# Kernel tuning notes

Hardware: AMD Instinct MI355X
Metric: run time of the kernel (lower is better)

The kernel has to match this reference:

```python
import jax, jax.numpy as jnp
import numpy as np
import math

H, W = 1024, 1280
NUM_CLASSES = 81  # 80 foreground + background
CENTER_VAR, SIZE_VAR = 0.1, 0.2
CONF_THR, NMS_THR = 0.01, 0.45
PRE_NMS_K, MAX_DET = 400, 100

def make_priors():
    strides_x = [32, 64, 128, 213, 320]
    strides_y = [32, 64, 128, 256, 512]
    fmx = [int(W / s) for s in strides_x]
    fmy = [int(H / s) for s in strides_y]
    expand = H / 256.0
    mins = [10 * expand, 62 * expand, 114 * expand, 166 * expand, 218 * expand]
    maxs = [62 * expand, 114 * expand, 166 * expand, 218 * expand, 270 * expand]
    ars = [[2, 3], [2, 3], [2, 3], [2], [2]]
    pri = []
    for k in range(5):
        for i in range(fmy[k]):
            for j in range(fmx[k]):
                cx = (j + 0.5) / fmx[k]
                cy = (i + 0.5) / fmy[k]
                pri.append([cx, cy, mins[k] / W, mins[k] / H])
                s = math.sqrt(mins[k] * maxs[k])
                pri.append([cx, cy, s / W, s / H])
                for r in ars[k]:
                    sr = math.sqrt(r)
                    pri.append([cx, cy, mins[k] * sr / W, mins[k] / sr / H])
                    pri.append([cx, cy, mins[k] / sr / W, mins[k] * sr / H])
    return np.clip(np.asarray(pri, np.float32), 0.0, 1.0)  # [P,4] center form

def setup_inputs():
    key = jax.random.key(0)
    k1, k2 = jax.random.split(key)
    pri = jnp.asarray(make_priors())  # [10208, 4]
    P = pri.shape[0]
    return {
        "cls_logits": jax.random.normal(k1, (32, P, NUM_CLASSES), jnp.float32),
        "bbox_pred": jax.random.normal(k2, (32, P, 4), jnp.float32) * 0.5,
        "priors": pri,
    }

def _decode(loc, priors):
    # convert_locations_to_boxes: center-form decode with variances
    c = loc[..., :2] * CENTER_VAR * priors[..., 2:] + priors[..., :2]
    s = jnp.exp(loc[..., 2:] * SIZE_VAR) * priors[..., 2:]
    # center_form_to_corner_form
    return jnp.concatenate([c - s * 0.5, c + s * 0.5], axis=-1)

def _iou(a, b):
    lt = jnp.maximum(a[:, None, :2], b[None, :, :2])
    rb = jnp.minimum(a[:, None, 2:], b[None, :, 2:])
    wh = jnp.clip(rb - lt, 0.0)
    inter = wh[..., 0] * wh[..., 1]
    ar = (a[:, 2] - a[:, 0]) * (a[:, 3] - a[:, 1])
    br = (b[:, 2] - b[:, 0]) * (b[:, 3] - b[:, 1])
    return inter / (ar[:, None] + br[None, :] - inter + 1e-9)

def _post_one(scores, boxes):
    # scores: [P, C] softmax probs, boxes: [P, 4] corner form in [0,1]
    C = scores.shape[1]
    fg = scores[:, 1:]  # drop background
    bx = boxes * jnp.asarray([W, H, W, H], boxes.dtype)  # scale to image coords
    topv, topi = jax.lax.top_k(fg.reshape(-1), PRE_NMS_K)  # pre-NMS candidates
    prior_idx = topi // (C - 1)
    cls = topi % (C - 1) + 1
    cb = bx[prior_idx]  # [K,4]
    # class-aware (batched) NMS: offset boxes by class so classes never overlap
    off = cls.astype(bx.dtype)[:, None] * float(max(H, W) + 1)
    ob = cb + off
    iou = _iou(ob, ob)  # [K,K]
    keep0 = topv > CONF_THR
    idx = jnp.arange(PRE_NMS_K)
    def body(keep, i):
        sup = (iou[i] > NMS_THR) & (idx > i) & keep[i]
        return keep & ~sup, None
    keep, _ = jax.lax.scan(body, keep0, jnp.arange(PRE_NMS_K))
    sc = jnp.where(keep, topv, 0.0)
    fv, fi = jax.lax.top_k(sc, MAX_DET)
    return cb[fi], cls[fi], fv  # boxes [100,4], labels [100], scores [100]

def reference(cls_logits, bbox_pred, priors):
    scores = jax.nn.softmax(cls_logits, axis=2)  # [B,P,C]
    boxes = _decode(bbox_pred, priors)           # [B,P,4]
    return jax.vmap(_post_one)(scores, boxes)
```

## Files before the change

kernel.cpp:

```cpp
#include <hip/hip_runtime.h>


#define BATCH   32
#define NCLS    81
#define CM1     80
#define KPRE    400
#define MAXDET  100
#define NBINS   4096
#define CAP     32768
#define THRESH  0.06f
#define CONFT   0.01f
#define NMST    0.45f
#define OFFMUL  1281.0f
#define WD      1280.0f
#define HT      1024.0f

#define SPB     256
#define HALF    128

#define OFF_CNT   0u
#define ZERO_BYTES 128u
#define OFF_CAND  1024u
#define OFF_TOPV  8389632u
#define OFF_CLS   8440832u
#define OFF_BOX   8492032u
#define OFF_SUP   8696832u

__global__ __launch_bounds__(256, 3) void k_score(const float* __restrict__ logits,
                                                  unsigned int* __restrict__ cnt,
                                                  uint2* __restrict__ cand, int P) {
    int b = blockIdx.y;
    int p0 = blockIdx.x * SPB;
    int npb = min(SPB, P - p0);
    int t = threadIdx.x;
    __shared__ float tile[HALF * NCLS];
    __shared__ unsigned int blk_cnt, blk_base;

    if (t == 0) blk_cnt = 0;

    float x[NCLS];
    int half = t >> 7;
    int lt = t & (HALF - 1);

    for (int h = 0; h < 2; ++h) {
        int nh = min(HALF, npb - h * HALF);
        if (nh > 0) {
            const float4* g4 = (const float4*)(logits + ((size_t)b * P + p0 + h * HALF) * NCLS);
            float4* t4 = (float4*)tile;
            int nv4 = (nh * NCLS) >> 2;
            for (int i = t; i < nv4; i += 256) t4[i] = g4[i];
        }
        __syncthreads();
        if (half == h && lt < nh) {
            const float* row = &tile[lt * NCLS];
            #pragma unroll
            for (int c = 0; c < NCLS; ++c) x[c] = row[c];
        }
        __syncthreads();
    }

    bool active = (t < npb);
    float mx = 0.f, s = 0.f, thr = 0.f;
    unsigned int mycnt = 0, myoff = 0;
    if (active) {
        float m0 = x[0], m1 = x[1], m2 = x[2], m3 = x[3];
        #pragma unroll
        for (int c = 4; c + 3 < NCLS; c += 4) {
            m0 = fmaxf(m0, x[c]);     m1 = fmaxf(m1, x[c + 1]);
            m2 = fmaxf(m2, x[c + 2]); m3 = fmaxf(m3, x[c + 3]);
        }
        mx = fmaxf(fmaxf(fmaxf(m0, m1), fmaxf(m2, m3)), x[NCLS - 1]);
        s = 0.0f;
        #pragma unroll
        for (int c = 0; c < NCLS; ++c) s = __fadd_rn(s, expf(__fsub_rn(x[c], mx)));
        thr = mx + logf(THRESH * s) - 1e-3f;
        #pragma unroll
        for (int c = 1; c < NCLS; ++c) mycnt += (x[c] > thr) ? 1u : 0u;
        if (mycnt) myoff = atomicAdd(&blk_cnt, mycnt);
    }
    __syncthreads();
    if (t == 0) blk_base = atomicAdd(&cnt[b], blk_cnt);
    __syncthreads();

    if (active && mycnt) {
        unsigned int pos = blk_base + myoff;
        unsigned int baseIdx = (unsigned int)(p0 + t) * CM1;
        #pragma unroll
        for (int c = 1; c < NCLS; ++c) {
            float xv = x[c];
            if (xv > thr) {
                float pr = __fdiv_rn(expf(__fsub_rn(xv, mx)), s);
                if (pos < CAP)
                    cand[(size_t)b * CAP + pos] = make_uint2(__float_as_uint(pr),
                                                             baseIdx + (unsigned)(c - 1));
                pos++;
            }
        }
    }
}

__global__ __launch_bounds__(256) void k_select(const unsigned int* __restrict__ cnt,
                                                const uint2* __restrict__ cand,
                                                const float* __restrict__ bbox,
                                                const float* __restrict__ priors,
                                                float* __restrict__ topv,
                                                unsigned int* __restrict__ clsA,
                                                float* __restrict__ boxA, int P) {
    int b = blockIdx.x;
    int tid = threadIdx.x;
    __shared__ unsigned int lh[NBINS];
    __shared__ unsigned long long keys[2048];
    __shared__ unsigned int sh_bstar, sh_M;

    for (int i = tid; i < NBINS; i += 256) lh[i] = 0u;
    if (tid == 0) sh_M = 0;
    __syncthreads();

    unsigned int n = min(cnt[b], (unsigned)CAP);
    for (unsigned int j = tid; j < n; j += 256) {
        unsigned int bits = cand[(size_t)b * CAP + j].x;
        atomicAdd(&lh[bits >> 19], 1u);
    }
    __syncthreads();

    if (tid < 64) {
        int lane = tid;
        unsigned int bsum = 0;
        for (int m = 0; m < 64; ++m) { int mm = (m + lane) & 63; bsum += lh[lane * 64 + mm]; }
        unsigned int S = bsum;
        for (int off = 1; off < 64; off <<= 1) {
            unsigned int o = __shfl(S, min(lane + off, 63));
            if (lane + off < 64) S += o;
        }
        unsigned int Sn = __shfl(S, min(lane + 1, 63)); if (lane == 63) Sn = 0;
        bool cond = (S >= KPRE) && (Sn < KPRE);
        unsigned long long bal = __ballot(cond);
        int Ls = (bal == 0) ? 0 : (__ffsll((long long)bal) - 1);
        unsigned int coarse = __shfl(Sn, Ls);
        unsigned int T = lh[Ls * 64 + lane];
        for (int off = 1; off < 64; off <<= 1) {
            unsigned int o = __shfl(T, min(lane + off, 63));
            if (lane + off < 64) T += o;
        }
        unsigned int Tn = __shfl(T, min(lane + 1, 63)); if (lane == 63) Tn = 0;
        bool cond2 = (coarse + T >= KPRE) && (coarse + Tn < KPRE);
        unsigned long long bal2 = __ballot(cond2);
        int Ms = (bal2 == 0) ? 0 : (__ffsll((long long)bal2) - 1);
        if (lane == 0) sh_bstar = (unsigned)(Ls * 64 + Ms);
    }
    __syncthreads();
    unsigned int bstar = sh_bstar;

    for (unsigned int j = tid; j < n; j += 256) {
        uint2 cd = cand[(size_t)b * CAP + j];
        if ((cd.x >> 19) >= bstar) {
            unsigned int pos = atomicAdd(&sh_M, 1u);
            if (pos < 2048) keys[pos] = ((unsigned long long)cd.x << 32) | (unsigned int)(~cd.y);
        }
    }
    __syncthreads();
    unsigned int M = min(sh_M, 2048u);
    unsigned int S2 = 512; while (S2 < M) S2 <<= 1;
    for (unsigned int i = M + tid; i < S2; i += 256) keys[i] = 0ull;
    __syncthreads();

    for (unsigned int k = 2; k <= S2; k <<= 1) {
        for (unsigned int j = k >> 1; j > 0; j >>= 1) {
            for (unsigned int i = tid; i < S2; i += 256) {
                unsigned int pi = i ^ j;
                if (pi > i) {
                    unsigned long long a = keys[i], bb = keys[pi];
                    bool sw = ((i & k) == 0) ? (a < bb) : (a > bb);
                    if (sw) { keys[i] = bb; keys[pi] = a; }
                }
            }
            __syncthreads();
        }
    }

    for (int k2 = tid; k2 < KPRE; k2 += 256) {
        unsigned long long key = keys[k2];
        unsigned int bits = (unsigned int)(key >> 32);
        unsigned int idx = ~((unsigned int)key);
        float val, x1, y1, x2, y2; unsigned int cc;
        if (bits == 0u) { val = 0.f; x1 = y1 = x2 = y2 = 0.f; cc = 0u; }
        else {
            val = __uint_as_float(bits);
            unsigned int prior = idx / CM1;
            cc = idx - prior * CM1 + 1u;
            const float* lp = bbox + ((size_t)b * P + prior) * 4;
            const float* pp = priors + (size_t)prior * 4;
            float cx = __fadd_rn(__fmul_rn(__fmul_rn(lp[0], 0.1f), pp[2]), pp[0]);
            float cy = __fadd_rn(__fmul_rn(__fmul_rn(lp[1], 0.1f), pp[3]), pp[1]);
            float sw = __fmul_rn(expf(__fmul_rn(lp[2], 0.2f)), pp[2]);
            float sh = __fmul_rn(expf(__fmul_rn(lp[3], 0.2f)), pp[3]);
            x1 = __fmul_rn(__fsub_rn(cx, __fmul_rn(sw, 0.5f)), WD);
            y1 = __fmul_rn(__fsub_rn(cy, __fmul_rn(sh, 0.5f)), HT);
            x2 = __fmul_rn(__fadd_rn(cx, __fmul_rn(sw, 0.5f)), WD);
            y2 = __fmul_rn(__fadd_rn(cy, __fmul_rn(sh, 0.5f)), HT);
        }
        size_t o = (size_t)b * KPRE + k2;
        topv[o] = val; clsA[o] = cc;
        boxA[o * 4 + 0] = x1; boxA[o * 4 + 1] = y1; boxA[o * 4 + 2] = x2; boxA[o * 4 + 3] = y2;
    }
}

__global__ __launch_bounds__(512) void k_iou(const float* __restrict__ boxA,
                                             const unsigned int* __restrict__ clsA,
                                             unsigned long long* __restrict__ sup) {
    int b = blockIdx.x;
    int w = blockIdx.y;
    int tid = threadIdx.x;
    __shared__ float ob[KPRE][4];
    for (int k = tid; k < KPRE; k += 512) {
        size_t o = (size_t)b * KPRE + k;
        float off = __fmul_rn((float)clsA[o], OFFMUL);
        ob[k][0] = __fadd_rn(boxA[o * 4 + 0], off);
        ob[k][1] = __fadd_rn(boxA[o * 4 + 1], off);
        ob[k][2] = __fadd_rn(boxA[o * 4 + 2], off);
        ob[k][3] = __fadd_rn(boxA[o * 4 + 3], off);
    }
    __syncthreads();
    int i = tid;
    if (i >= KPRE) return;
    float a0 = ob[i][0], a1 = ob[i][1], a2 = ob[i][2], a3 = ob[i][3];
    float ar = __fmul_rn(__fsub_rn(a2, a0), __fsub_rn(a3, a1));
    unsigned long long m = 0ull;
    int jmax = min(64, KPRE - w * 64);
    for (int jb = 0; jb < jmax; ++jb) {
        int j = w * 64 + jb;
        float ltx = fmaxf(a0, ob[j][0]), lty = fmaxf(a1, ob[j][1]);
        float rbx = fminf(a2, ob[j][2]), rby = fminf(a3, ob[j][3]);
        float wd = fmaxf(__fsub_rn(rbx, ltx), 0.0f);
        float ht = fmaxf(__fsub_rn(rby, lty), 0.0f);
        float inter = __fmul_rn(wd, ht);
        float br = __fmul_rn(__fsub_rn(ob[j][2], ob[j][0]), __fsub_rn(ob[j][3], ob[j][1]));
        float den = __fadd_rn(__fsub_rn(__fadd_rn(ar, br), inter), 1e-9f);
        float iou = __fdiv_rn(inter, den);
        if (j > i && iou > NMST) m |= (1ull << jb);
    }
    sup[((size_t)b * KPRE + i) * 7 + w] = m;
}

__global__ __launch_bounds__(128) void k_nms(const unsigned long long* __restrict__ sup,
                                             const float* __restrict__ topv,
                                             const unsigned int* __restrict__ clsA,
                                             const float* __restrict__ boxA,
                                             float* __restrict__ out) {
    int b = blockIdx.x;
    int tid = threadIdx.x;
    __shared__ unsigned long long ls[KPRE * 7];
    __shared__ float tv[KPRE];
    __shared__ unsigned long long keepw[7];
    for (int w = tid; w < KPRE * 7; w += 128) ls[w] = sup[(size_t)b * KPRE * 7 + w];
    for (int k = tid; k < KPRE; k += 128) tv[k] = topv[(size_t)b * KPRE + k];
    if (tid < 7) keepw[tid] = 0ull;
    __syncthreads();
    for (int k = tid; k < KPRE; k += 128)
        if (tv[k] > CONFT) atomicOr(&keepw[k >> 6], 1ull << (k & 63));
    __syncthreads();

    if (tid < 64) {
        unsigned long long q0 = keepw[0], q1 = keepw[1], q2 = keepw[2], q3 = keepw[3],
                           q4 = keepw[4], q5 = keepw[5], q6 = keepw[6];
#define NMSW(W, QW, NB)                                                           \
        for (int bi = 0; bi < NB; ++bi) {                                         \
            if ((QW >> bi) & 1ull) {                                              \
                const unsigned long long* rr = &ls[(unsigned)(W * 64 + bi) * 7u]; \
                q0 &= ~rr[0]; q1 &= ~rr[1]; q2 &= ~rr[2]; q3 &= ~rr[3];           \
                q4 &= ~rr[4]; q5 &= ~rr[5]; q6 &= ~rr[6];                         \
            }                                                                     \
        }
        NMSW(0, q0, 64) NMSW(1, q1, 64) NMSW(2, q2, 64) NMSW(3, q3, 64)
        NMSW(4, q4, 64) NMSW(5, q5, 64) NMSW(6, q6, 16)
#undef NMSW
        if (tid == 0) {
            keepw[0] = q0; keepw[1] = q1; keepw[2] = q2; keepw[3] = q3;
            keepw[4] = q4; keepw[5] = q5; keepw[6] = q6;
        }
    }
    __syncthreads();

    int tot = 0;
    for (int t = 0; t < 7; ++t) tot += __popcll(keepw[t]);
    for (int k = tid; k < KPRE; k += 128) {
        int w = k >> 6, bi = k & 63;
        unsigned long long kw = keepw[w];
        int before = __popcll(kw & ((1ull << bi) - 1ull));
        for (int t = 0; t < w; ++t) before += __popcll(keepw[t]);
        bool kept = (kw >> bi) & 1ull;
        int rank = kept ? before : (tot + (k - before));
        if (rank < MAXDET) {
            size_t so = (size_t)b * KPRE + k;
            size_t dof = (size_t)b * MAXDET + rank;
            out[dof * 4 + 0] = boxA[so * 4 + 0];
            out[dof * 4 + 1] = boxA[so * 4 + 1];
            out[dof * 4 + 2] = boxA[so * 4 + 2];
            out[dof * 4 + 3] = boxA[so * 4 + 3];
            out[(size_t)BATCH * MAXDET * 4 + dof] = (float)clsA[so];
            out[(size_t)BATCH * MAXDET * 5 + dof] = kept ? tv[k] : 0.0f;
        }
    }
}

extern "C" void kernel_launch(void* const* d_in, const int* in_sizes, int n_in,
                              void* d_out, int out_size, void* d_ws, size_t ws_size,
                              hipStream_t stream) {
    (void)n_in; (void)out_size; (void)ws_size;
    const float* logits = (const float*)d_in[0];
    const float* bbox   = (const float*)d_in[1];
    const float* priors = (const float*)d_in[2];
    int P = in_sizes[2] / 4;

    char* ws = (char*)d_ws;
    unsigned int* cnt  = (unsigned int*)(ws + OFF_CNT);
    uint2* cand        = (uint2*)(ws + OFF_CAND);
    float* topv        = (float*)(ws + OFF_TOPV);
    unsigned int* clsA = (unsigned int*)(ws + OFF_CLS);
    float* boxA        = (float*)(ws + OFF_BOX);
    unsigned long long* sup = (unsigned long long*)(ws + OFF_SUP);

    hipMemsetAsync(ws, 0, ZERO_BYTES, stream);

    dim3 g1((P + SPB - 1) / SPB, BATCH);
    k_score<<<g1, 256, 0, stream>>>(logits, cnt, cand, P);
    k_select<<<BATCH, 256, 0, stream>>>(cnt, cand, bbox, priors, topv, clsA, boxA, P);
    k_iou<<<dim3(BATCH, 7), 512, 0, stream>>>(boxA, clsA, sup);
    k_nms<<<BATCH, 128, 0, stream>>>(sup, topv, clsA, boxA, (float*)d_out);
}
```

Before: 317.2 us.

## Score rows per wave from LDS and stage candidates for coalesced writes

Rewrites the softmax/threshold scoring kernel. Each of four 64-row phases is loaded into shared memory, and one wave computes on it directly from LDS instead of holding 81 logits in registers per thread. Candidates go into an LDS buffer through shared atomics, and the wave reserves global space with a single atomic before writing them out contiguously. The aim is lower register pressure (launch bound raised to 4 blocks per CU) and coalesced candidate stores. In exchange, only one wave per block computes in each phase between barriers, and candidate order within a batch changes.

Measured after the change: 417.0 us. +31.5%, slower.

```diff
diff --git a/kernel.cpp b/kernel.cpp
--- a/kernel.cpp
+++ b/kernel.cpp
@@ -16,7 +16,9 @@
 #define HT      1024.0f
 
 #define SPB     256
-#define HALF    128
+#define RPP     64
+#define NPH     4
+#define WBUF_N  1024
 
 #define OFF_CNT   0u
 #define ZERO_BYTES 128u
@@ -26,76 +28,74 @@
 #define OFF_BOX   8492032u
 #define OFF_SUP   8696832u
 
-__global__ __launch_bounds__(256, 3) void k_score(const float* __restrict__ logits,
+__global__ __launch_bounds__(256, 4) void k_score(const float* __restrict__ logits,
                                                   unsigned int* __restrict__ cnt,
                                                   uint2* __restrict__ cand, int P) {
     int b = blockIdx.y;
     int p0 = blockIdx.x * SPB;
-    int npb = min(SPB, P - p0);
     int t = threadIdx.x;
-    __shared__ float tile[HALF * NCLS];
-    __shared__ unsigned int blk_cnt, blk_base;
-
-    if (t == 0) blk_cnt = 0;
-
-    float x[NCLS];
-    int half = t >> 7;
-    int lt = t & (HALF - 1);
-
-    for (int h = 0; h < 2; ++h) {
-        int nh = min(HALF, npb - h * HALF);
+    int wave = t >> 6, lane = t & 63;
+    __shared__ float tile[RPP * NCLS];
+    __shared__ uint2 wbuf[WBUF_N];
+    __shared__ unsigned int wcnt;
+
+    for (int h = 0; h < NPH; ++h) {
+        int r0 = p0 + h * RPP;
+        int nh = min(RPP, P - r0);
         if (nh > 0) {
-            const float4* g4 = (const float4*)(logits + ((size_t)b * P + p0 + h * HALF) * NCLS);
+            const float4* g4 = (const float4*)(logits + ((size_t)b * P + r0) * NCLS);
             float4* t4 = (float4*)tile;
             int nv4 = (nh * NCLS) >> 2;
             for (int i = t; i < nv4; i += 256) t4[i] = g4[i];
         }
         __syncthreads();
-        if (half == h && lt < nh) {
-            const float* row = &tile[lt * NCLS];
+
+        if (wave == h && nh > 0) {
+            if (lane == 0) wcnt = 0;
+            bool act = lane < nh;
+            const float* x = &tile[lane * NCLS];
+            float mx = 0.f, s = 0.f, thr = 0.f;
+            unsigned int mycnt = 0;
+            if (act) {
+                float m0 = x[0], m1 = x[1], m2 = x[2], m3 = x[3];
+                #pragma unroll
+                for (int c = 4; c + 3 < NCLS; c += 4) {
+                    m0 = fmaxf(m0, x[c]);     m1 = fmaxf(m1, x[c + 1]);
+                    m2 = fmaxf(m2, x[c + 2]); m3 = fmaxf(m3, x[c + 3]);
+                }
+                mx = fmaxf(fmaxf(fmaxf(m0, m1), fmaxf(m2, m3)), x[NCLS - 1]);
+                s = 0.0f;
+                #pragma unroll
+                for (int c = 0; c < NCLS; ++c) s = __fadd_rn(s, expf(__fsub_rn(x[c], mx)));
+                thr = mx + logf(THRESH * s) - 1e-3f;
+            }
+            if (act) {
+                unsigned int baseIdx = (unsigned int)(r0 + lane) * CM1;
+                for (int c = 1; c < NCLS; ++c) {
+                    float xv = x[c];
+                    if (xv > thr) {
+                        float pr = __fdiv_rn(expf(__fsub_rn(xv, mx)), s);
+                        unsigned int slot = atomicAdd(&wcnt, 1u);
+                        if (slot < WBUF_N)
+                            wbuf[slot] = make_uint2(__float_as_uint(pr),
+                                                    baseIdx + (unsigned)(c - 1));
+                        ++mycnt;
+                    }
+                }
+            }
+            unsigned int tot = mycnt;
             #pragma unroll
-            for (int c = 0; c < NCLS; ++c) x[c] = row[c];
+            for (int d = 32; d; d >>= 1) tot += __shfl_down(tot, d);
+            tot = __shfl(tot, 0);
+            unsigned int base = 0;
+            if (lane == 0 && tot) base = atomicAdd(&cnt[b], tot);
+            base = __shfl(base, 0);
+            for (unsigned int i = lane; i < tot && i < WBUF_N; i += 64) {
+                unsigned int pos = base + i;
+                if (pos < CAP) cand[(size_t)b * CAP + pos] = wbuf[i];
+            }
         }
         __syncthreads();
-    }
-
-    bool active = (t < npb);
-    float mx = 0.f, s = 0.f, thr = 0.f;
-    unsigned int mycnt = 0, myoff = 0;
-    if (active) {
-        float m0 = x[0], m1 = x[1], m2 = x[2], m3 = x[3];
-        #pragma unroll
-        for (int c = 4; c + 3 < NCLS; c += 4) {
-            m0 = fmaxf(m0, x[c]);     m1 = fmaxf(m1, x[c + 1]);
-            m2 = fmaxf(m2, x[c + 2]); m3 = fmaxf(m3, x[c + 3]);
-        }
-        mx = fmaxf(fmaxf(fmaxf(m0, m1), fmaxf(m2, m3)), x[NCLS - 1]);
-        s = 0.0f;
-        #pragma unroll
-        for (int c = 0; c < NCLS; ++c) s = __fadd_rn(s, expf(__fsub_rn(x[c], mx)));
-        thr = mx + logf(THRESH * s) - 1e-3f;
-        #pragma unroll
-        for (int c = 1; c < NCLS; ++c) mycnt += (x[c] > thr) ? 1u : 0u;
-        if (mycnt) myoff = atomicAdd(&blk_cnt, mycnt);
-    }
-    __syncthreads();
-    if (t == 0) blk_base = atomicAdd(&cnt[b], blk_cnt);
-    __syncthreads();
-
-    if (active && mycnt) {
-        unsigned int pos = blk_base + myoff;
-        unsigned int baseIdx = (unsigned int)(p0 + t) * CM1;
-        #pragma unroll
-        for (int c = 1; c < NCLS; ++c) {
-            float xv = x[c];
-            if (xv > thr) {
-                float pr = __fdiv_rn(expf(__fsub_rn(xv, mx)), s);
-                if (pos < CAP)
-                    cand[(size_t)b * CAP + pos] = make_uint2(__float_as_uint(pr),
-                                                             baseIdx + (unsigned)(c - 1));
-                pos++;
-            }
-        }
     }
 }
 
```
